# Kernel optimization log

Measured on AMD Instinct MI355X. Metric: run time of the kernel, lower is better.

## Reference

```python
import jax, jax.numpy as jnp
import numpy as np

CHANNELS = 512
NUM_HEADS = 4
GROUPS = 32
EPS = 1e-5


def setup_inputs() -> dict:
    key = jax.random.key(0)
    ks = jax.random.split(key, 7)
    C = CHANNELS
    x = jax.random.normal(ks[0], (16, C, 32, 32), dtype=jnp.float32)
    norm_w = jnp.ones((C,), dtype=jnp.float32)
    norm_b = jnp.zeros((C,), dtype=jnp.float32)
    qkv_w = jax.random.normal(ks[1], (3 * C, C), dtype=jnp.float32) * (C ** -0.5)
    qkv_b = jnp.zeros((3 * C,), dtype=jnp.float32)
    proj_w = jax.random.normal(ks[2], (C, C), dtype=jnp.float32) * (C ** -0.5)
    proj_b = jnp.zeros((C,), dtype=jnp.float32)
    return {"x": x, "norm_w": norm_w, "norm_b": norm_b,
            "qkv_w": qkv_w, "qkv_b": qkv_b,
            "proj_w": proj_w, "proj_b": proj_b}


def reference(x, norm_w, norm_b, qkv_w, qkv_b, proj_w, proj_b):
    B, C, H, W = x.shape
    heads = NUM_HEADS
    hd = C // heads  # head dim
    N = H * W

    # GroupNorm(32, C): normalize over (C/32, H, W) per group, then per-channel affine
    xg = x.reshape(B, GROUPS, -1)
    mu = jnp.mean(xg, axis=-1, keepdims=True)
    var = jnp.var(xg, axis=-1, keepdims=True)
    h = ((xg - mu) * jax.lax.rsqrt(var + EPS)).reshape(B, C, H, W)
    h = h * norm_w[None, :, None, None] + norm_b[None, :, None, None]

    # 1x1 conv qkv: [B,C,H,W] -> [B,3C,H,W]
    qkv = jnp.einsum('oc,bchw->bohw', qkv_w, h) + qkv_b[None, :, None, None]
    qkv = qkv.reshape(B, 3, heads, hd, N)
    q, k, v = qkv[:, 0], qkv[:, 1], qkv[:, 2]  # each [B, heads, hd, N]

    scale = hd ** -0.5
    attn = jnp.einsum('bhcn,bhcm->bhnm', q, k) * scale  # [B, heads, N, N]
    attn = jax.nn.softmax(attn, axis=-1)
    h = jnp.einsum('bhnm,bhcm->bhcn', attn, v).reshape(B, C, H, W)

    # 1x1 conv proj + residual
    h = jnp.einsum('oc,bchw->bohw', proj_w, h) + proj_b[None, :, None, None]
    return x + h
```

## Files before the change

### kernel.cpp

```cpp
#include <hip/hip_runtime.h>

typedef __bf16 v8bf __attribute__((ext_vector_type(8)));
typedef float  v4f  __attribute__((ext_vector_type(4)));
typedef unsigned short u16;

__device__ __forceinline__ u16 f2bf(float f){
  __bf16 h = (__bf16)f;
  union { __bf16 h; u16 u; } c; c.h = h; return c.u;
}
__device__ __forceinline__ v4f v4zero(){ v4f z; z[0]=0.f; z[1]=0.f; z[2]=0.f; z[3]=0.f; return z; }

#define MFMA16(a,b,c) __builtin_amdgcn_mfma_f32_16x16x32_bf16((a),(b),(c),0,0,0)

__device__ __forceinline__ void gl_lds16(const u16* g, u16* l){
  __builtin_amdgcn_global_load_lds((const __attribute__((address_space(1))) void*)g,
                                   (__attribute__((address_space(3))) void*)l, 16, 0, 0);
}

__global__ __launch_bounds__(256) void cvt_kernel(const float* __restrict__ src, u16* __restrict__ dst, int n){
  int i = (blockIdx.x*256 + threadIdx.x)*4;
  if (i < n){
    float4 v = *(const float4*)(src + i);
    ushort4 o;
    o.x = f2bf(v.x); o.y = f2bf(v.y); o.z = f2bf(v.z); o.w = f2bf(v.w);
    *(ushort4*)(dst + i) = o;
  }
}

__global__ __launch_bounds__(256) void gn_stats_kernel(const float* __restrict__ x, float* __restrict__ stats){
  const float* base = x + (size_t)blockIdx.x * 16384;
  float s = 0.f, ss = 0.f;
  #pragma unroll
  for (int it = 0; it < 16; ++it){
    float4 v = *(const float4*)(base + it*1024 + threadIdx.x*4);
    s  += v.x + v.y + v.z + v.w;
    ss += v.x*v.x + v.y*v.y + v.z*v.z + v.w*v.w;
  }
  #pragma unroll
  for (int off = 32; off > 0; off >>= 1){ s += __shfl_down(s, off); ss += __shfl_down(ss, off); }
  __shared__ float red[8];
  int w = threadIdx.x >> 6;
  if ((threadIdx.x & 63) == 0){ red[w] = s; red[4+w] = ss; }
  __syncthreads();
  if (threadIdx.x == 0){
    float S  = red[0]+red[1]+red[2]+red[3];
    float SS = red[4]+red[5]+red[6]+red[7];
    float mean = S * (1.f/16384.f);
    float var  = SS * (1.f/16384.f) - mean*mean;
    stats[blockIdx.x*2]   = mean;
    stats[blockIdx.x*2+1] = rsqrtf(var + 1e-5f);
  }
}

__global__ __launch_bounds__(256) void gn_apply_kernel(const float* __restrict__ x, const float* __restrict__ nw,
                                                       const float* __restrict__ nb, const float* __restrict__ stats,
                                                       u16* __restrict__ h_t){
  __shared__ u16 tile[32*520];
  int b = blockIdx.y, n0 = blockIdx.x*32, tid = threadIdx.x;
  int cr = tid >> 2, nn = (tid & 3)*8;
  #pragma unroll
  for (int p = 0; p < 8; ++p){
    int c = p*64 + cr;
    const float* px = x + (size_t)(b*512 + c)*1024 + n0 + nn;
    float4 u0 = *(const float4*)(px);
    float4 u1 = *(const float4*)(px + 4);
    int g = c >> 4;
    float mean = stats[(b*32+g)*2], rstd = stats[(b*32+g)*2+1];
    float wv = nw[c], bv = nb[c];
    float vals[8] = {u0.x,u0.y,u0.z,u0.w,u1.x,u1.y,u1.z,u1.w};
    #pragma unroll
    for (int e = 0; e < 8; ++e)
      tile[(nn+e)*520 + c] = f2bf((vals[e] - mean)*rstd*wv + bv);
  }
  __syncthreads();
  #pragma unroll
  for (int p = 0; p < 8; ++p){
    int n  = p*4 + (tid >> 6);
    int c0 = (tid & 63)*8;
    *(int4*)(h_t + ((size_t)b*1024 + n0 + n)*512 + c0) = *(int4*)(tile + n*520 + c0);
  }
}

__global__ __launch_bounds__(256,2) void gemm_qkv_kernel(
    const u16* __restrict__ A,
    const u16* __restrict__ B,
    const float* __restrict__ bias,
    u16* __restrict__ qk_t, u16* __restrict__ v_ws)
{
  __shared__ u16 smem[24576];
  u16* As = smem;
  u16* Bs = smem + 128*64;
  const int tid = threadIdx.x, w = tid>>6, lane = tid&63, col = lane&15, quad = lane>>4;
  const int m0 = blockIdx.y*128;
  const int n0 = blockIdx.x*256;
  const int b  = blockIdx.z;
  const int lr8 = lane>>3;
  const int gsw = ((lane&7) ^ lr8)*8;
  const u16* Ag = A + ((size_t)b*1024 + m0 + w*32 + lr8)*512 + gsw;
  const u16* Bg = B + (size_t)(n0 + w*64 + lr8)*512 + gsw;
  u16* ldsA = As + (w*32)*64;
  u16* ldsB = Bs + (w*64)*64;
  const int mw = (w&1)*64, nw = (w>>1)*128;
  const int csw = col&7;

  v4f acc[4][8];
  #pragma unroll
  for (int i=0;i<4;++i)
    #pragma unroll
    for (int j=0;j<8;++j) acc[i][j] = v4zero();

  for (int kt = 0; kt < 512; kt += 64){
    #pragma unroll
    for (int p = 0; p < 4; ++p)
      gl_lds16(Ag + (size_t)(p*8)*512 + kt, ldsA + p*512);
    #pragma unroll
    for (int p = 0; p < 8; ++p)
      gl_lds16(Bg + (size_t)(p*8)*512 + kt, ldsB + p*512);
    __syncthreads();
    #pragma unroll
    for (int kh = 0; kh < 2; ++kh){
      const int fs = ((kh*4 + quad) ^ csw)*8;
      v8bf a[4], bb[8];
      #pragma unroll
      for (int i = 0; i < 4; ++i) a[i]  = *(const v8bf*)(As + (mw+i*16+col)*64 + fs);
      #pragma unroll
      for (int j = 0; j < 8; ++j) bb[j] = *(const v8bf*)(Bs + (nw+j*16+col)*64 + fs);
      #pragma unroll
      for (int i = 0; i < 4; ++i)
        #pragma unroll
        for (int j = 0; j < 8; ++j)
          acc[i][j] = MFMA16(a[i], bb[j], acc[i][j]);
    }
    __syncthreads();
  }

  float bc[8];
  #pragma unroll
  for (int j = 0; j < 8; ++j)
    bc[j] = bias[n0 + nw + j*16 + col];

  if (n0 < 1024){
    u16* Cs = smem + w*(64*72);
    #pragma unroll
    for (int half = 0; half < 2; ++half){
      #pragma unroll
      for (int i = 0; i < 4; ++i)
        #pragma unroll
        for (int jj = 0; jj < 4; ++jj)
          #pragma unroll
          for (int r = 0; r < 4; ++r)
            Cs[(i*16+quad*4+r)*72 + jj*16+col] = f2bf(acc[i][half*4+jj][r] + bc[half*4+jj]);
      u16* dst = qk_t + (size_t)b*1024*1024;
      #pragma unroll
      for (int p = 0; p < 8; ++p){
        int rl = p*8 + (lane>>3), cl = (lane&7)*8;
        *(int4*)(dst + (size_t)(m0+mw+rl)*1024 + n0+nw+half*64+cl) = *(int4*)(Cs + rl*72 + cl);
      }
    }
  } else {
    u16* Ct = smem + w*(64*80);
    #pragma unroll
    for (int half = 0; half < 2; ++half){
      #pragma unroll
      for (int i = 0; i < 4; ++i)
        #pragma unroll
        for (int jj = 0; jj < 4; ++jj)
          #pragma unroll
          for (int r = 0; r < 4; ++r)
            Ct[(jj*16+col)*80 + i*16+quad*4+r] = f2bf(acc[i][half*4+jj][r] + bc[half*4+jj]);
      u16* dst = v_ws + (size_t)b*512*1024;
      #pragma unroll
      for (int p = 0; p < 8; ++p){
        int rl = p*8 + (lane>>3), cl = (lane&7)*8;
        *(int4*)(dst + (size_t)(n0-1024 + nw + half*64 + rl)*1024 + m0+mw+cl) = *(int4*)(Ct + rl*80 + cl);
      }
    }
  }
}

__global__ __launch_bounds__(256,2) void gemm_bt_kernel(
    const u16* __restrict__ A, long long sA,
    const u16* __restrict__ B, long long sB,
    u16* __restrict__ Cbf, float* __restrict__ Cf, long long sC,
    const float* __restrict__ bias_row,
    const float* __restrict__ bias_col,
    const float* __restrict__ residf, long long sR,
    int M, int N, int K)
{
  __shared__ u16 smem[18432];
  u16* As = smem;
  u16* Bs = smem + 128*64;
  const int tid = threadIdx.x, w = tid>>6, lane = tid&63, col = lane&15, quad = lane>>4;
  const int m0 = blockIdx.y*128, n0 = blockIdx.x*128;
  const int lr8 = lane>>3;
  const int gsw = ((lane&7) ^ lr8)*8;
  const u16* Ag = A + (size_t)blockIdx.z*sA + (size_t)(m0 + w*32 + lr8)*K + gsw;
  const u16* Bg = B + (size_t)blockIdx.z*sB + (size_t)(n0 + w*32 + lr8)*K + gsw;
  u16* ldsA = As + (w*32)*64;
  u16* ldsB = Bs + (w*32)*64;
  const int mw = (w&1)*64, nw = (w>>1)*64;
  const int csw = col&7;

  v4f acc[4][4];
  #pragma unroll
  for (int i=0;i<4;++i)
    #pragma unroll
    for (int j=0;j<4;++j) acc[i][j] = v4zero();

  for (int kt = 0; kt < K; kt += 64){
    #pragma unroll
    for (int p = 0; p < 4; ++p){
      gl_lds16(Ag + (size_t)(p*8)*K + kt, ldsA + p*512);
      gl_lds16(Bg + (size_t)(p*8)*K + kt, ldsB + p*512);
    }
    __syncthreads();
    #pragma unroll
    for (int kh = 0; kh < 2; ++kh){
      const int fs = ((kh*4 + quad) ^ csw)*8;
      v8bf a[4], bb[4];
      #pragma unroll
      for (int i = 0; i < 4; ++i) a[i]  = *(const v8bf*)(As + (mw+i*16+col)*64 + fs);
      #pragma unroll
      for (int j = 0; j < 4; ++j) bb[j] = *(const v8bf*)(Bs + (nw+j*16+col)*64 + fs);
      #pragma unroll
      for (int i = 0; i < 4; ++i)
        #pragma unroll
        for (int j = 0; j < 4; ++j)
          acc[i][j] = MFMA16(a[i], bb[j], acc[i][j]);
    }
    __syncthreads();
  }

  float br[4][4], bc[4];
  #pragma unroll
  for (int i = 0; i < 4; ++i)
    #pragma unroll
    for (int r = 0; r < 4; ++r)
      br[i][r] = bias_row ? bias_row[m0+mw+i*16+quad*4+r] : 0.f;
  #pragma unroll
  for (int j = 0; j < 4; ++j)
    bc[j] = bias_col ? bias_col[n0+nw+j*16+col] : 0.f;

  if (Cf){
    float* Cb = Cf + (size_t)blockIdx.z*sC;
    const float* Rb = residf ? residf + (size_t)blockIdx.z*sR : nullptr;
    #pragma unroll
    for (int i = 0; i < 4; ++i)
      #pragma unroll
      for (int r = 0; r < 4; ++r){
        int row = m0+mw+i*16+quad*4+r;
        #pragma unroll
        for (int j = 0; j < 4; ++j){
          size_t goff = (size_t)row*N + n0+nw+j*16+col;
          float val = acc[i][j][r] + br[i][r] + bc[j];
          if (Rb) val += Rb[goff];
          Cb[goff] = val;
        }
      }
  } else {
    u16* Cs = smem + w*(64*72);
    #pragma unroll
    for (int i = 0; i < 4; ++i)
      #pragma unroll
      for (int j = 0; j < 4; ++j)
        #pragma unroll
        for (int r = 0; r < 4; ++r)
          Cs[(i*16+quad*4+r)*72 + j*16+col] = f2bf(acc[i][j][r] + br[i][r] + bc[j]);
    __syncthreads();
    u16* Cb = Cbf + (size_t)blockIdx.z*sC;
    #pragma unroll
    for (int p = 0; p < 8; ++p){
      int rl = p*8 + (lane>>3), cl = (lane&7)*8;
      size_t goff = (size_t)(m0+mw+rl)*N + n0+nw+cl;
      *(int4*)(Cb + goff) = *(int4*)(Cs + rl*72 + cl);
    }
  }
}

__global__ __launch_bounds__(256,2) void attn_kernel(const u16* __restrict__ qk, const u16* __restrict__ vv,
                                                     u16* __restrict__ outp){
  __shared__ u16 smem[25600];
  u16* Ks = smem;
  u16* Vs = smem + 8192;
  u16* Ps = smem + 8192 + 9216;
  const int id = blockIdx.x;
  const int qt = id >> 6, bh = id & 63, b = bh >> 2, h = bh & 3;
  const int n0 = qt*128;
  const int tid = threadIdx.x, w = tid>>6, lane = tid&63, col = lane&15, quad = lane>>4;
  const size_t bq = (size_t)b*1024*1024;
  const float scale2 = 0.12751742f;

  if (tid < 128){
    int r = 128 + (tid>>3);
    int pat = (r == 128) ? (int)0x3F803F80u : 0;
    int4 v; v.x = pat; v.y = pat; v.z = pat; v.w = pat;
    *(int4*)(Vs + r*64 + (tid&7)*8) = v;
  }

  v8bf aq[2][4];
  #pragma unroll
  for (int i = 0; i < 2; ++i)
    #pragma unroll
    for (int kk = 0; kk < 4; ++kk)
      aq[i][kk] = *(const v8bf*)(qk + bq + (size_t)(n0 + w*32 + i*16 + col)*1024 + h*128 + kk*32 + quad*8);

  v4f o[2][9];
  #pragma unroll
  for (int i=0;i<2;++i)
    #pragma unroll
    for (int j=0;j<9;++j) o[i][j] = v4zero();

  const int krow = w*4 + (lane>>4);
  const int kgr  = (lane&15) ^ (krow&7);
  const u16* kg_base = qk + bq + (size_t)krow*1024 + 512 + h*128 + kgr*8;
  u16* kl_base = Ks + (w*4)*128;
  const int vrow = w*8 + (lane>>3);
  const int vgr  = (lane&7) ^ (vrow&7);
  const u16* vg_base = vv + ((size_t)b*512 + h*128 + vrow)*1024 + vgr*8;
  u16* vl_base = Vs + (w*8)*64;

  for (int mt = 0; mt < 1024; mt += 64){
    #pragma unroll
    for (int p = 0; p < 4; ++p)
      gl_lds16(kg_base + (size_t)(mt + p*16)*1024, kl_base + p*16*128);
    #pragma unroll
    for (int p = 0; p < 4; ++p)
      gl_lds16(vg_base + (size_t)(p*32)*1024 + mt, vl_base + p*32*64);
    __syncthreads();

    v4f s[2][4];
    #pragma unroll
    for (int i=0;i<2;++i)
      #pragma unroll
      for (int j=0;j<4;++j) s[i][j] = v4zero();
    #pragma unroll
    for (int kk = 0; kk < 4; ++kk){
      v8bf bk[4];
      #pragma unroll
      for (int j = 0; j < 4; ++j){
        int r = j*16 + col;
        int g = (kk*4 + quad) ^ (r&7);
        bk[j] = *(const v8bf*)(Ks + (r<<7) + (g<<3));
      }
      #pragma unroll
      for (int i = 0; i < 2; ++i)
        #pragma unroll
        for (int j = 0; j < 4; ++j)
          s[i][j] = MFMA16(aq[i][kk], bk[j], s[i][j]);
    }

    #pragma unroll
    for (int i = 0; i < 2; ++i)
      #pragma unroll
      for (int j = 0; j < 4; ++j)
        #pragma unroll
        for (int r = 0; r < 4; ++r){
          int rr = w*32 + i*16 + quad*4 + r;
          int m  = j*16 + col;
          int key = (rr ^ (rr>>3)) & 7;
          Ps[(rr<<6) + ((((m>>3) ^ key))<<3) + (m&7)] = f2bf(exp2f(s[i][j][r]*scale2));
        }

    #pragma unroll
    for (int kk = 0; kk < 2; ++kk){
      v8bf ap[2];
      #pragma unroll
      for (int i = 0; i < 2; ++i){
        int rr = w*32 + i*16 + col;
        int key = (rr ^ (rr>>3)) & 7;
        int g = (kk*4 + quad) ^ key;
        ap[i] = *(const v8bf*)(Ps + (rr<<6) + (g<<3));
      }
      #pragma unroll
      for (int j = 0; j < 9; ++j){
        int vr = j*16 + col;
        int g = (kk*4 + quad) ^ (vr&7);
        v8bf bv = *(const v8bf*)(Vs + (vr<<6) + (g<<3));
        #pragma unroll
        for (int i = 0; i < 2; ++i) o[i][j] = MFMA16(ap[i], bv, o[i][j]);
      }
    }
    __syncthreads();
  }

  #pragma unroll
  for (int i = 0; i < 2; ++i)
    #pragma unroll
    for (int r = 0; r < 4; ++r){
      float l = __shfl(o[i][8][r], quad<<4);
      float inv = 1.f / l;
      #pragma unroll
      for (int j = 0; j < 8; ++j) o[i][j][r] *= inv;
    }

  #pragma unroll
  for (int i = 0; i < 2; ++i)
    #pragma unroll
    for (int j = 0; j < 8; ++j)
      #pragma unroll
      for (int r = 0; r < 4; ++r){
        int rr = w*32 + i*16 + quad*4 + r;
        int c  = j*16 + col;
        smem[(rr<<7) + ((((c>>3) ^ (rr&7))<<3)) + (c&7)] = f2bf(o[i][j][r]);
      }
  __syncthreads();
  #pragma unroll
  for (int p = 0; p < 8; ++p){
    int nr = p*16 + (tid>>4);
    int gc = (tid&15) ^ (nr&7);
    *(int4*)(outp + ((size_t)b*1024 + n0 + nr)*512 + h*128 + ((tid&15)<<3)) =
      *(int4*)(smem + (nr<<7) + (gc<<3));
  }
}

extern "C" void kernel_launch(void* const* d_in, const int* in_sizes, int n_in,
                              void* d_out, int out_size, void* d_ws, size_t ws_size,
                              hipStream_t stream){
  const float* x      = (const float*)d_in[0];
  const float* norm_w = (const float*)d_in[1];
  const float* norm_b = (const float*)d_in[2];
  const float* qkv_w  = (const float*)d_in[3];
  const float* qkv_b  = (const float*)d_in[4];
  const float* proj_w = (const float*)d_in[5];
  const float* proj_b = (const float*)d_in[6];
  float* out = (float*)d_out;

  u16* h_t   = (u16*)d_ws;
  u16* qk_t  = h_t  + (size_t)16*1024*512;
  u16* v_ws  = qk_t + (size_t)16*1024*1024;
  u16* wq_bf = v_ws + (size_t)16*512*1024;
  u16* wp_bf = wq_bf + (size_t)1536*512;
  float* stats = (float*)(wp_bf + (size_t)512*512);
  u16* attnout = h_t;

  cvt_kernel<<<768, 256, 0, stream>>>(qkv_w, wq_bf, 1536*512);
  cvt_kernel<<<256, 256, 0, stream>>>(proj_w, wp_bf, 512*512);
  gn_stats_kernel<<<512, 256, 0, stream>>>(x, stats);
  gn_apply_kernel<<<dim3(32,16), 256, 0, stream>>>(x, norm_w, norm_b, stats, h_t);

  gemm_qkv_kernel<<<dim3(6,8,16), 256, 0, stream>>>(h_t, wq_bf, qkv_b, qk_t, v_ws);

  attn_kernel<<<512, 256, 0, stream>>>(qk_t, v_ws, attnout);

  gemm_bt_kernel<<<dim3(8,4,16), 256, 0, stream>>>(
      wp_bf, 0, attnout, (long long)1024*512,
      nullptr, out, (long long)512*1024, proj_b, nullptr, x, (long long)512*1024, 512, 1024, 512);
}
```

Measured before the change: 218.8 us.

## Double-buffer LDS in GEMM and attention kernels, compute softmax row sums in registers

```diff
diff --git a/kernel.cpp b/kernel.cpp
--- a/kernel.cpp
+++ b/kernel.cpp
@@ -88,20 +88,16 @@
     u16* __restrict__ qk_t, u16* __restrict__ v_ws)
 {
   __shared__ u16 smem[24576];
-  u16* As = smem;
-  u16* Bs = smem + 128*64;
   const int tid = threadIdx.x, w = tid>>6, lane = tid&63, col = lane&15, quad = lane>>4;
   const int m0 = blockIdx.y*128;
   const int n0 = blockIdx.x*256;
   const int b  = blockIdx.z;
-  const int lr8 = lane>>3;
-  const int gsw = ((lane&7) ^ lr8)*8;
-  const u16* Ag = A + ((size_t)b*1024 + m0 + w*32 + lr8)*512 + gsw;
-  const u16* Bg = B + (size_t)(n0 + w*64 + lr8)*512 + gsw;
-  u16* ldsA = As + (w*32)*64;
-  u16* ldsB = Bs + (w*64)*64;
+  const int lr = lane>>2;
+  const int gsw = ((lane&3) ^ (lr&3))*8;
+  const u16* Ag = A + ((size_t)b*1024 + m0 + w*32 + lr)*512 + gsw;
+  const u16* Bg = B + (size_t)(n0 + w*64 + lr)*512 + gsw;
   const int mw = (w&1)*64, nw = (w>>1)*128;
-  const int csw = col&7;
+  const int fsw = (quad ^ (col&3))*8;
 
   v4f acc[4][8];
   #pragma unroll
@@ -109,30 +105,40 @@
     #pragma unroll
     for (int j=0;j<8;++j) acc[i][j] = v4zero();
 
-  for (int kt = 0; kt < 512; kt += 64){
-    #pragma unroll
-    for (int p = 0; p < 4; ++p)
-      gl_lds16(Ag + (size_t)(p*8)*512 + kt, ldsA + p*512);
-    #pragma unroll
-    for (int p = 0; p < 8; ++p)
-      gl_lds16(Bg + (size_t)(p*8)*512 + kt, ldsB + p*512);
+  {
+    u16* Ab = smem + (w*32)*32;
+    u16* Bb = smem + 4096 + (w*64)*32;
+    #pragma unroll
+    for (int p = 0; p < 2; ++p) gl_lds16(Ag + (size_t)(p*16)*512, Ab + p*512);
+    #pragma unroll
+    for (int p = 0; p < 4; ++p) gl_lds16(Bg + (size_t)(p*16)*512, Bb + p*512);
+  }
+
+  for (int kt = 0; kt < 16; ++kt){
     __syncthreads();
-    #pragma unroll
-    for (int kh = 0; kh < 2; ++kh){
-      const int fs = ((kh*4 + quad) ^ csw)*8;
-      v8bf a[4], bb[8];
-      #pragma unroll
-      for (int i = 0; i < 4; ++i) a[i]  = *(const v8bf*)(As + (mw+i*16+col)*64 + fs);
-      #pragma unroll
-      for (int j = 0; j < 8; ++j) bb[j] = *(const v8bf*)(Bs + (nw+j*16+col)*64 + fs);
-      #pragma unroll
-      for (int i = 0; i < 4; ++i)
-        #pragma unroll
-        for (int j = 0; j < 8; ++j)
-          acc[i][j] = MFMA16(a[i], bb[j], acc[i][j]);
-    }
-    __syncthreads();
-  }
+    if (kt < 15){
+      u16* Ab = smem + ((kt+1)&1)*12288 + (w*32)*32;
+      u16* Bb = smem + ((kt+1)&1)*12288 + 4096 + (w*64)*32;
+      int ko = (kt+1)*32;
+      #pragma unroll
+      for (int p = 0; p < 2; ++p) gl_lds16(Ag + (size_t)(p*16)*512 + ko, Ab + p*512);
+      #pragma unroll
+      for (int p = 0; p < 4; ++p) gl_lds16(Bg + (size_t)(p*16)*512 + ko, Bb + p*512);
+    }
+    const u16* As = smem + (kt&1)*12288;
+    const u16* Bs = As + 4096;
+    v8bf a[4], bb[8];
+    #pragma unroll
+    for (int i = 0; i < 4; ++i) a[i]  = *(const v8bf*)(As + (mw+i*16+col)*32 + fsw);
+    #pragma unroll
+    for (int j = 0; j < 8; ++j) bb[j] = *(const v8bf*)(Bs + (nw+j*16+col)*32 + fsw);
+    #pragma unroll
+    for (int i = 0; i < 4; ++i)
+      #pragma unroll
+      for (int j = 0; j < 8; ++j)
+        acc[i][j] = MFMA16(a[i], bb[j], acc[i][j]);
+  }
+  __syncthreads();
 
   float bc[8];
   #pragma unroll
@@ -187,19 +193,16 @@
     const float* __restrict__ residf, long long sR,
     int M, int N, int K)
 {
-  __shared__ u16 smem[18432];
-  u16* As = smem;
-  u16* Bs = smem + 128*64;
+  __shared__ u16 smem[32768];
   const int tid = threadIdx.x, w = tid>>6, lane = tid&63, col = lane&15, quad = lane>>4;
   const int m0 = blockIdx.y*128, n0 = blockIdx.x*128;
   const int lr8 = lane>>3;
   const int gsw = ((lane&7) ^ lr8)*8;
   const u16* Ag = A + (size_t)blockIdx.z*sA + (size_t)(m0 + w*32 + lr8)*K + gsw;
   const u16* Bg = B + (size_t)blockIdx.z*sB + (size_t)(n0 + w*32 + lr8)*K + gsw;
-  u16* ldsA = As + (w*32)*64;
-  u16* ldsB = Bs + (w*32)*64;
   const int mw = (w&1)*64, nw = (w>>1)*64;
   const int csw = col&7;
+  const int nt = K >> 6;
 
   v4f acc[4][4];
   #pragma unroll
@@ -207,13 +210,30 @@
     #pragma unroll
     for (int j=0;j<4;++j) acc[i][j] = v4zero();
 
-  for (int kt = 0; kt < K; kt += 64){
+  {
+    u16* Ab = smem + (w*32)*64;
+    u16* Bb = smem + 8192 + (w*32)*64;
     #pragma unroll
     for (int p = 0; p < 4; ++p){
-      gl_lds16(Ag + (size_t)(p*8)*K + kt, ldsA + p*512);
-      gl_lds16(Bg + (size_t)(p*8)*K + kt, ldsB + p*512);
-    }
+      gl_lds16(Ag + (size_t)(p*8)*K, Ab + p*512);
+      gl_lds16(Bg + (size_t)(p*8)*K, Bb + p*512);
+    }
+  }
+
+  for (int kt = 0; kt < nt; ++kt){
     __syncthreads();
+    if (kt+1 < nt){
+      u16* Ab = smem + ((kt+1)&1)*16384 + (w*32)*64;
+      u16* Bb = smem + ((kt+1)&1)*16384 + 8192 + (w*32)*64;
+      int ko = (kt+1)*64;
+      #pragma unroll
+      for (int p = 0; p < 4; ++p){
+        gl_lds16(Ag + (size_t)(p*8)*K + ko, Ab + p*512);
+        gl_lds16(Bg + (size_t)(p*8)*K + ko, Bb + p*512);
+      }
+    }
+    const u16* As = smem + (kt&1)*16384;
+    const u16* Bs = As + 8192;
     #pragma unroll
     for (int kh = 0; kh < 2; ++kh){
       const int fs = ((kh*4 + quad) ^ csw)*8;
@@ -228,8 +248,8 @@
         for (int j = 0; j < 4; ++j)
           acc[i][j] = MFMA16(a[i], bb[j], acc[i][j]);
     }
-    __syncthreads();
-  }
+  }
+  __syncthreads();
 
   float br[4][4], bc[4];
   #pragma unroll
@@ -279,10 +299,10 @@
 
 __global__ __launch_bounds__(256,2) void attn_kernel(const u16* __restrict__ qk, const u16* __restrict__ vv,
                                                      u16* __restrict__ outp){
-  __shared__ u16 smem[25600];
+  __shared__ u16 smem[32768];
   u16* Ks = smem;
   u16* Vs = smem + 8192;
-  u16* Ps = smem + 8192 + 9216;
+  u16* Ps = smem + 8192 + 16384;
   const int id = blockIdx.x;
   const int qt = id >> 6, bh = id & 63, b = bh >> 2, h = bh & 3;
   const int n0 = qt*128;
@@ -290,13 +310,6 @@
   const size_t bq = (size_t)b*1024*1024;
   const float scale2 = 0.12751742f;
 
-  if (tid < 128){
-    int r = 128 + (tid>>3);
-    int pat = (r == 128) ? (int)0x3F803F80u : 0;
-    int4 v; v.x = pat; v.y = pat; v.z = pat; v.w = pat;
-    *(int4*)(Vs + r*64 + (tid&7)*8) = v;
-  }
-
   v8bf aq[2][4];
   #pragma unroll
   for (int i = 0; i < 2; ++i)
@@ -304,11 +317,14 @@
     for (int kk = 0; kk < 4; ++kk)
       aq[i][kk] = *(const v8bf*)(qk + bq + (size_t)(n0 + w*32 + i*16 + col)*1024 + h*128 + kk*32 + quad*8);
 
-  v4f o[2][9];
+  v4f o[2][8];
   #pragma unroll
   for (int i=0;i<2;++i)
     #pragma unroll
-    for (int j=0;j<9;++j) o[i][j] = v4zero();
+    for (int j=0;j<8;++j) o[i][j] = v4zero();
+  float lsum[8];
+  #pragma unroll
+  for (int r=0;r<8;++r) lsum[r] = 0.f;
 
   const int krow = w*4 + (lane>>4);
   const int kgr  = (lane&15) ^ (krow&7);
@@ -317,15 +333,16 @@
   const int vrow = w*8 + (lane>>3);
   const int vgr  = (lane&7) ^ (vrow&7);
   const u16* vg_base = vv + ((size_t)b*512 + h*128 + vrow)*1024 + vgr*8;
-  u16* vl_base = Vs + (w*8)*64;
-
-  for (int mt = 0; mt < 1024; mt += 64){
-    #pragma unroll
-    for (int p = 0; p < 4; ++p)
-      gl_lds16(kg_base + (size_t)(mt + p*16)*1024, kl_base + p*16*128);
-    #pragma unroll
-    for (int p = 0; p < 4; ++p)
-      gl_lds16(vg_base + (size_t)(p*32)*1024 + mt, vl_base + p*32*64);
+
+  #pragma unroll
+  for (int p = 0; p < 4; ++p)
+    gl_lds16(kg_base + (size_t)(p*16)*1024, kl_base + p*16*128);
+  #pragma unroll
+  for (int p = 0; p < 4; ++p)
+    gl_lds16(vg_base + (size_t)(p*32)*1024, Vs + (w*8 + p*32)*64);
+
+  for (int t = 0; t < 16; ++t){
+    const int mt = t*64;
     __syncthreads();
 
     v4f s[2][4];
@@ -348,46 +365,77 @@
         for (int j = 0; j < 4; ++j)
           s[i][j] = MFMA16(aq[i][kk], bk[j], s[i][j]);
     }
+    __syncthreads();
+
+    if (t < 15){
+      int mt2 = mt + 64;
+      #pragma unroll
+      for (int p = 0; p < 4; ++p)
+        gl_lds16(kg_base + (size_t)(mt2 + p*16)*1024, kl_base + p*16*128);
+      u16* vl = Vs + (((t+1)&1)<<13) + (w*8)*64;
+      #pragma unroll
+      for (int p = 0; p < 4; ++p)
+        gl_lds16(vg_base + (size_t)(p*32)*1024 + mt2, vl + p*32*64);
+    }
 
     #pragma unroll
     for (int i = 0; i < 2; ++i)
       #pragma unroll
-      for (int j = 0; j < 4; ++j)
-        #pragma unroll
-        for (int r = 0; r < 4; ++r){
-          int rr = w*32 + i*16 + quad*4 + r;
-          int m  = j*16 + col;
-          int key = (rr ^ (rr>>3)) & 7;
-          Ps[(rr<<6) + ((((m>>3) ^ key))<<3) + (m&7)] = f2bf(exp2f(s[i][j][r]*scale2));
-        }
-
+      for (int r = 0; r < 4; ++r){
+        float p0 = __builtin_amdgcn_exp2f(s[i][0][r]*scale2);
+        float p1 = __builtin_amdgcn_exp2f(s[i][1][r]*scale2);
+        float p2 = __builtin_amdgcn_exp2f(s[i][2][r]*scale2);
+        float p3 = __builtin_amdgcn_exp2f(s[i][3][r]*scale2);
+        lsum[i*4+r] += (p0+p1) + (p2+p3);
+        int rr = w*32 + i*16 + quad*4 + r;
+        int key = (rr ^ (rr>>2)) & 7;
+        Ps[(rr<<6) + (((0 ^ key))<<3) + (col&7) + ((col>>3)? ((1^key)<<3)-((0^key)<<3) : 0)] = f2bf(p0);
+        Ps[(rr<<6) + ((((16*1+col)>>3) ^ key)<<3) + (col&7)] = f2bf(p1);
+        Ps[(rr<<6) + ((((16*2+col)>>3) ^ key)<<3) + (col&7)] = f2bf(p2);
+        Ps[(rr<<6) + ((((16*3+col)>>3) ^ key)<<3) + (col&7)] = f2bf(p3);
+      }
+    #pragma unroll
+    for (int i = 0; i < 2; ++i)
+      #pragma unroll
+      for (int r = 0; r < 4; ++r){
+        int rr = w*32 + i*16 + quad*4 + r;
+        int key = (rr ^ (rr>>2)) & 7;
+        float p0 = __builtin_amdgcn_exp2f(s[i][0][r]*scale2);
+        Ps[(rr<<6) + ((((col)>>3) ^ key)<<3) + (col&7)] = f2bf(p0);
+      }
+
+    const u16* Vc = Vs + ((t&1)<<13);
     #pragma unroll
     for (int kk = 0; kk < 2; ++kk){
       v8bf ap[2];
       #pragma unroll
       for (int i = 0; i < 2; ++i){
         int rr = w*32 + i*16 + col;
-        int key = (rr ^ (rr>>3)) & 7;
+        int key = (rr ^ (rr>>2)) & 7;
         int g = (kk*4 + quad) ^ key;
         ap[i] = *(const v8bf*)(Ps + (rr<<6) + (g<<3));
       }
       #pragma unroll
-      for (int j = 0; j < 9; ++j){
+      for (int j = 0; j < 8; ++j){
         int vr = j*16 + col;
         int g = (kk*4 + quad) ^ (vr&7);
-        v8bf bv = *(const v8bf*)(Vs + (vr<<6) + (g<<3));
+        v8bf bv = *(const v8bf*)(Vc + (vr<<6) + (g<<3));
         #pragma unroll
         for (int i = 0; i < 2; ++i) o[i][j] = MFMA16(ap[i], bv, o[i][j]);
       }
     }
-    __syncthreads();
-  }
+  }
+  __syncthreads();
 
   #pragma unroll
   for (int i = 0; i < 2; ++i)
     #pragma unroll
     for (int r = 0; r < 4; ++r){
-      float l = __shfl(o[i][8][r], quad<<4);
+      float l = lsum[i*4+r];
+      l += __shfl_xor(l, 1);
+      l += __shfl_xor(l, 2);
+      l += __shfl_xor(l, 4);
+      l += __shfl_xor(l, 8);
       float inv = 1.f / l;
       #pragma unroll
       for (int j = 0; j < 8; ++j) o[i][j][r] *= inv;
```

Result: no change. 215.7 us (-1.4%).
